# Optimization experiments

Hardware: AMD Instinct MI355X
Metric: run time of the kernel (lower is better)

The kernel has to match this reference:

```python
import jax, jax.numpy as jnp
import numpy as np

STD = 1.0  # components_std from cfg
LOG_2PI = float(np.log(2.0 * np.pi))


def setup_inputs() -> dict:
    key = jax.random.key(0)
    k1, k2, k3 = jax.random.split(key, 3)
    B, S, D, K = 256, 1024, 32, 512
    x = jax.random.normal(k1, (B, S, D), dtype=jnp.float32)
    logits = jax.random.normal(k2, (B, K), dtype=jnp.float32)
    # xavier_normal_ init on (K, D): std = sqrt(2 / (K + D))
    means = jax.random.normal(k3, (K, D), dtype=jnp.float32) * np.sqrt(2.0 / (K + D))
    return {"x": x, "logits": logits, "means": means}


def reference(x, logits, means):
    # x: [B, S, D], logits: [B, K], means: [K, D]
    D = x.shape[-1]
    log_mix = jax.nn.log_softmax(logits, axis=-1)  # [B, K] Categorical log-probs
    # squared distance ||x - mu||^2 via expansion (avoids [B,S,K,D] intermediate)
    x2 = jnp.sum(x * x, axis=-1)          # [B, S]
    m2 = jnp.sum(means * means, axis=-1)  # [K]
    xm = jnp.einsum('bsd,kd->bsk', x, means)  # [B, S, K]
    sq = x2[..., None] - 2.0 * xm + m2        # [B, S, K]
    inv_var = 1.0 / (STD * STD)
    log_norm = D * (jnp.log(jnp.float32(STD)) + 0.5 * LOG_2PI)
    comp_logpdf = -0.5 * inv_var * sq - log_norm  # [B, S, K] Independent-Normal logpdf
    # mixture log_prob = logsumexp over components; NLL = negative
    nll = -jax.nn.logsumexp(log_mix[:, None, :] + comp_logpdf, axis=-1)  # [B, S]
    return nll
```

## Files before the change

### kernel.cpp

```cpp
#include <hip/hip_runtime.h>
#include <math.h>

constexpr int Bc = 256, Sc = 1024, Dc = 32, Kc = 512;
constexpr int ST = 128;
constexpr float LOG2E    = 1.4426950408889634f;
constexpr float LN2      = 0.6931471805599453f;
constexpr float LOG_NORM = 29.40603306051f;

typedef __attribute__((ext_vector_type(4))) float f32x4;

#if __has_builtin(__builtin_amdgcn_exp2f)
#define EXP2F(v) __builtin_amdgcn_exp2f(v)
#else
#define EXP2F(v) exp2f(v)
#endif
#if __has_builtin(__builtin_amdgcn_logf)
#define LOG2F(v) __builtin_amdgcn_logf(v)
#else
#define LOG2F(v) log2f(v)
#endif

template <bool HI>
__device__ __forceinline__ int pkfp8(float a, float b, int old) {
    return __builtin_amdgcn_cvt_pk_fp8_f32(a, b, old, HI);
}

__device__ __forceinline__ int swz8(int row, int chunk) {
    return row * 32 + ((chunk ^ ((row >> 2) & 3)) << 3);
}

__global__ __launch_bounds__(256)
void gm_m2f8(const float* __restrict__ means,
             unsigned short* __restrict__ mf8, float* __restrict__ m2buf)
{
    const int t  = blockIdx.x * 256 + threadIdx.x;
    const float v0 = means[2 * t];
    const float v1 = means[2 * t + 1];
    mf8[t] = (unsigned short)(pkfp8<false>(v0, v1, 0) & 0xffff);
    float sq = v0 * v0 + v1 * v1;
    #pragma unroll
    for (int off = 1; off <= 8; off <<= 1) sq += __shfl_xor(sq, off);
    if ((threadIdx.x & 15) == 0) m2buf[t >> 4] = sq;
}

__global__ __launch_bounds__(256, 8)
void gm_main(const float* __restrict__ x, const float* __restrict__ logits,
             const float* __restrict__ m2buf, const unsigned short* __restrict__ mf8,
             float* __restrict__ out)
{
    __shared__ unsigned char mlds[Kc * 32];
    __shared__ float wlds[Kc];
    __shared__ float x2p[ST];
    __shared__ float red[8];

    const int tid  = threadIdx.x;
    const int lane = tid & 63;
    const int wid  = tid >> 6;
    const int b    = blockIdx.x >> 3;
    const int s0   = (blockIdx.x & 7) * ST;
    const int q    = lane >> 4;
    const int ln   = lane & 15;
    const int rw   = wid * 32;

    {
        const unsigned long long* src = (const unsigned long long*)mf8;
        #pragma unroll
        for (int j = 0; j < 8; ++j) {
            const int c = tid + j * 256;
            *(unsigned long long*)&mlds[swz8(c >> 2, c & 3)] = src[c];
        }
    }

    const float l0 = logits[b * Kc + tid];
    const float l1 = logits[b * Kc + tid + 256];
    wlds[tid]       = EXP2F((l0 - 0.5f * m2buf[tid])       * LOG2E);
    wlds[tid + 256] = EXP2F((l1 - 0.5f * m2buf[tid + 256]) * LOG2E);

    float mx = fmaxf(l0, l1);
    #pragma unroll
    for (int off = 32; off >= 1; off >>= 1) mx = fmaxf(mx, __shfl_xor(mx, off));
    if (lane == 0) red[wid] = mx;

    const int row0 = rw + ln, row1 = row0 + 16;
    long a0, a1;
    {
        const float4* xp0 = (const float4*)(x + ((size_t)b * Sc + s0 + row0) * Dc) + q * 2;
        float4 v0 = xp0[0], v1 = xp0[1];
        int2 A;
        A.x = pkfp8<false>(v0.x * LOG2E, v0.y * LOG2E, 0);
        A.x = pkfp8<true >(v0.z * LOG2E, v0.w * LOG2E, A.x);
        A.y = pkfp8<false>(v1.x * LOG2E, v1.y * LOG2E, 0);
        A.y = pkfp8<true >(v1.z * LOG2E, v1.w * LOG2E, A.y);
        a0 = *(const long*)&A;
        float p = v0.x*v0.x + v0.y*v0.y + v0.z*v0.z + v0.w*v0.w
                + v1.x*v1.x + v1.y*v1.y + v1.z*v1.z + v1.w*v1.w;
        p += __shfl_xor(p, 16); p += __shfl_xor(p, 32);
        if (q == 0) x2p[row0] = p;
    }
    {
        const float4* xp1 = (const float4*)(x + ((size_t)b * Sc + s0 + row1) * Dc) + q * 2;
        float4 u0 = xp1[0], u1 = xp1[1];
        int2 A;
        A.x = pkfp8<false>(u0.x * LOG2E, u0.y * LOG2E, 0);
        A.x = pkfp8<true >(u0.z * LOG2E, u0.w * LOG2E, A.x);
        A.y = pkfp8<false>(u1.x * LOG2E, u1.y * LOG2E, 0);
        A.y = pkfp8<true >(u1.z * LOG2E, u1.w * LOG2E, A.y);
        a1 = *(const long*)&A;
        float p = u0.x*u0.x + u0.y*u0.y + u0.z*u0.z + u0.w*u0.w
                + u1.x*u1.x + u1.y*u1.y + u1.z*u1.z + u1.w*u1.w;
        p += __shfl_xor(p, 16); p += __shfl_xor(p, 32);
        if (q == 0) x2p[row1] = p;
    }
    __syncthreads();

    const float mxb = fmaxf(fmaxf(red[0], red[1]), fmaxf(red[2], red[3]));
    float sm = EXP2F((l0 - mxb) * LOG2E) + EXP2F((l1 - mxb) * LOG2E);
    #pragma unroll
    for (int off = 32; off >= 1; off >>= 1) sm += __shfl_xor(sm, off);
    if (lane == 0) red[4 + wid] = sm;

    const int bbase = ln * 32 + ((q ^ ((ln >> 2) & 3)) << 3);
    const f32x4 zero = {0.f, 0.f, 0.f, 0.f};
    float acc0[4] = {0.f, 0.f, 0.f, 0.f};
    float acc1[4] = {0.f, 0.f, 0.f, 0.f};

    #pragma unroll 4
    for (int kt = 0; kt < 32; ++kt) {
        const long  bfr = *(const long*)&mlds[bbase + kt * 512];
        const float wv  = wlds[kt * 16 + ln];
        f32x4 d0 = __builtin_amdgcn_mfma_f32_16x16x32_fp8_fp8(a0, bfr, zero, 0, 0, 0);
        f32x4 d1 = __builtin_amdgcn_mfma_f32_16x16x32_fp8_fp8(a1, bfr, zero, 0, 0, 0);
        #pragma unroll
        for (int r = 0; r < 4; ++r) {
            acc0[r] = fmaf(wv, EXP2F(d0[r]), acc0[r]);
            acc1[r] = fmaf(wv, EXP2F(d1[r]), acc1[r]);
        }
    }
    __syncthreads();
    const float lse  = mxb + LN2 * LOG2F(red[4] + red[5] + red[6] + red[7]);
    const float base = LOG_NORM + lse;

    #pragma unroll
    for (int r = 0; r < 4; ++r) {
        float s0v = acc0[r], s1v = acc1[r];
        s0v += __shfl_xor(s0v, 1); s0v += __shfl_xor(s0v, 2);
        s0v += __shfl_xor(s0v, 4); s0v += __shfl_xor(s0v, 8);
        s1v += __shfl_xor(s1v, 1); s1v += __shfl_xor(s1v, 2);
        s1v += __shfl_xor(s1v, 4); s1v += __shfl_xor(s1v, 8);
        if (ln == 0) {
            const int r0 = rw + q * 4 + r;
            const int r1 = r0 + 16;
            out[(size_t)b * Sc + s0 + r0] = 0.5f * x2p[r0] + base - LN2 * LOG2F(s0v);
            out[(size_t)b * Sc + s0 + r1] = 0.5f * x2p[r1] + base - LN2 * LOG2F(s1v);
        }
    }
}

extern "C" void kernel_launch(void* const* d_in, const int* in_sizes, int n_in,
                              void* d_out, int out_size, void* d_ws, size_t ws_size,
                              hipStream_t stream) {
    const float* x      = (const float*)d_in[0];
    const float* logits = (const float*)d_in[1];
    const float* means  = (const float*)d_in[2];
    float* out = (float*)d_out;
    (void)in_sizes; (void)n_in; (void)out_size; (void)ws_size;

    unsigned short* mf8   = (unsigned short*)d_ws;
    float*          m2buf = (float*)((char*)d_ws + 16384);

    hipLaunchKernelGGL(gm_m2f8, dim3(32), dim3(256), 0, stream, means, mf8, m2buf);
    hipLaunchKernelGGL(gm_main, dim3(Bc * (Sc / ST)), dim3(256), 0, stream,
                       x, logits, m2buf, mf8, out);
}
```

Before: 90.02 us.

## Replace exp2 with Schraudolph bit-trick exponent and transpose LDS layout for wide loads

Replaces the hardware exp2 and weight multiply in the inner loop with a Schraudolph-style approximation: the log-weight is pre-folded into a biased integer exponent, so each term becomes one FMA, a float-to-int convert and a bit reinterpret. The means fp8 tile and the weights are also relaid out in LDS (transposed with a new XOR swizzle), so each lane fetches four k-tiles' B fragments and weights with 16-byte loads instead of per-tile 8-byte and scalar loads. This cuts transcendental and LDS instruction count, at the cost of a piecewise-linear exponential approximation with a few percent relative error, and a risk of integer overflow or wrap for large arguments.

```diff
diff --git a/kernel.cpp b/kernel.cpp
--- a/kernel.cpp
+++ b/kernel.cpp
@@ -7,7 +7,11 @@
 constexpr float LN2      = 0.6931471805599453f;
 constexpr float LOG_NORM = 29.40603306051f;
 
+constexpr float FE_SCALE = 8388608.0f;
+constexpr float FE_BIAS  = 1064992048.0f;
+
 typedef __attribute__((ext_vector_type(4))) float f32x4;
+typedef __attribute__((ext_vector_type(2))) long longx2;
 
 #if __has_builtin(__builtin_amdgcn_exp2f)
 #define EXP2F(v) __builtin_amdgcn_exp2f(v)
@@ -25,10 +29,6 @@
     return __builtin_amdgcn_cvt_pk_fp8_f32(a, b, old, HI);
 }
 
-__device__ __forceinline__ int swz8(int row, int chunk) {
-    return row * 32 + ((chunk ^ ((row >> 2) & 3)) << 3);
-}
-
 __global__ __launch_bounds__(256)
 void gm_m2f8(const float* __restrict__ means,
              unsigned short* __restrict__ mf8, float* __restrict__ m2buf)
@@ -48,8 +48,8 @@
              const float* __restrict__ m2buf, const unsigned short* __restrict__ mf8,
              float* __restrict__ out)
 {
-    __shared__ unsigned char mlds[Kc * 32];
-    __shared__ float wlds[Kc];
+    __shared__ __align__(16) unsigned char mldsT[Kc * 32];
+    __shared__ float wT[16 * 44];
     __shared__ float x2p[ST];
     __shared__ float red[8];
 
@@ -66,15 +66,20 @@
         const unsigned long long* src = (const unsigned long long*)mf8;
         #pragma unroll
         for (int j = 0; j < 8; ++j) {
-            const int c = tid + j * 256;
-            *(unsigned long long*)&mlds[swz8(c >> 2, c & 3)] = src[c];
+            const int c   = tid + j * 256;
+            const int ktc = c >> 6;
+            const int ch  = ((c >> 2) & 15) * 4 + (c & 3);
+            *(unsigned long long*)&mldsT[(ch << 8) + ((ktc << 3) ^ (((ch >> 2) & 7) << 4))]
+                = src[c];
         }
     }
 
     const float l0 = logits[b * Kc + tid];
     const float l1 = logits[b * Kc + tid + 256];
-    wlds[tid]       = EXP2F((l0 - 0.5f * m2buf[tid])       * LOG2E);
-    wlds[tid + 256] = EXP2F((l1 - 0.5f * m2buf[tid + 256]) * LOG2E);
+    wT[(tid & 15) * 44 + (tid >> 4)]      =
+        fmaf((l0 - 0.5f * m2buf[tid])       * LOG2E, FE_SCALE, FE_BIAS);
+    wT[(tid & 15) * 44 + (tid >> 4) + 16] =
+        fmaf((l1 - 0.5f * m2buf[tid + 256]) * LOG2E, FE_SCALE, FE_BIAS);
 
     float mx = fmaxf(l0, l1);
     #pragma unroll
@@ -119,21 +124,47 @@
     for (int off = 32; off >= 1; off >>= 1) sm += __shfl_xor(sm, off);
     if (lane == 0) red[4 + wid] = sm;
 
-    const int bbase = ln * 32 + ((q ^ ((ln >> 2) & 3)) << 3);
+    const int ch   = ln * 4 + q;
+    const int bbT  = ch << 8;
+    const int swzv = (ln & 7) << 4;
+    const int ln44 = ln * 44;
     const f32x4 zero = {0.f, 0.f, 0.f, 0.f};
     float acc0[4] = {0.f, 0.f, 0.f, 0.f};
     float acc1[4] = {0.f, 0.f, 0.f, 0.f};
 
-    #pragma unroll 4
-    for (int kt = 0; kt < 32; ++kt) {
-        const long  bfr = *(const long*)&mlds[bbase + kt * 512];
-        const float wv  = wlds[kt * 16 + ln];
-        f32x4 d0 = __builtin_amdgcn_mfma_f32_16x16x32_fp8_fp8(a0, bfr, zero, 0, 0, 0);
-        f32x4 d1 = __builtin_amdgcn_mfma_f32_16x16x32_fp8_fp8(a1, bfr, zero, 0, 0, 0);
-        #pragma unroll
-        for (int r = 0; r < 4; ++r) {
-            acc0[r] = fmaf(wv, EXP2F(d0[r]), acc0[r]);
-            acc1[r] = fmaf(wv, EXP2F(d1[r]), acc1[r]);
+    #pragma unroll 2
+    for (int kt = 0; kt < 32; kt += 4) {
+        const longx2 p01 = *(const longx2*)&mldsT[bbT + (((kt    ) << 3) ^ swzv)];
+        const longx2 p23 = *(const longx2*)&mldsT[bbT + (((kt + 2) << 3) ^ swzv)];
+        const float4 wv4 = *(const float4*)&wT[ln44 + kt];
+        f32x4 d0, d1;
+        d0 = __builtin_amdgcn_mfma_f32_16x16x32_fp8_fp8(a0, p01.x, zero, 0, 0, 0);
+        d1 = __builtin_amdgcn_mfma_f32_16x16x32_fp8_fp8(a1, p01.x, zero, 0, 0, 0);
+        #pragma unroll
+        for (int r = 0; r < 4; ++r) {
+            acc0[r] += __int_as_float((int)fmaf(d0[r], FE_SCALE, wv4.x));
+            acc1[r] += __int_as_float((int)fmaf(d1[r], FE_SCALE, wv4.x));
+        }
+        d0 = __builtin_amdgcn_mfma_f32_16x16x32_fp8_fp8(a0, p01.y, zero, 0, 0, 0);
+        d1 = __builtin_amdgcn_mfma_f32_16x16x32_fp8_fp8(a1, p01.y, zero, 0, 0, 0);
+        #pragma unroll
+        for (int r = 0; r < 4; ++r) {
+            acc0[r] += __int_as_float((int)fmaf(d0[r], FE_SCALE, wv4.y));
+            acc1[r] += __int_as_float((int)fmaf(d1[r], FE_SCALE, wv4.y));
+        }
+        d0 = __builtin_amdgcn_mfma_f32_16x16x32_fp8_fp8(a0, p23.x, zero, 0, 0, 0);
+        d1 = __builtin_amdgcn_mfma_f32_16x16x32_fp8_fp8(a1, p23.x, zero, 0, 0, 0);
+        #pragma unroll
+        for (int r = 0; r < 4; ++r) {
+            acc0[r] += __int_as_float((int)fmaf(d0[r], FE_SCALE, wv4.z));
+            acc1[r] += __int_as_float((int)fmaf(d1[r], FE_SCALE, wv4.z));
+        }
+        d0 = __builtin_amdgcn_mfma_f32_16x16x32_fp8_fp8(a0, p23.y, zero, 0, 0, 0);
+        d1 = __builtin_amdgcn_mfma_f32_16x16x32_fp8_fp8(a1, p23.y, zero, 0, 0, 0);
+        #pragma unroll
+        for (int r = 0; r < 4; ++r) {
+            acc0[r] += __int_as_float((int)fmaf(d0[r], FE_SCALE, wv4.w));
+            acc1[r] += __int_as_float((int)fmaf(d1[r], FE_SCALE, wv4.w));
         }
     }
     __syncthreads();
```

New measurement: 93.00 us. +3.3%, slower.
